# Kernel optimization log

Hardware: AMD Instinct MI355X
Metric: run time of the kernel (lower is better)

The kernel has to match this reference:

```python
import jax, jax.numpy as jnp
import numpy as np

N_NODES = 50000
N_EDGES = 800000
HIDDEN = 128
N_REL = 64
NUM_HEADS = 8
HEAD_DIM = HIDDEN // NUM_HEADS


def setup_inputs() -> dict:
    key = jax.random.key(0)
    ks = jax.random.split(key, 20)
    s = 0.05
    inp = {
        "x": jax.random.normal(ks[0], (N_NODES, HIDDEN), dtype=jnp.float32),
        "timestamps": jax.random.uniform(ks[1], (N_NODES,), dtype=jnp.float32),
        "src": jax.random.randint(ks[2], (N_EDGES,), 0, N_NODES),
        "dst": jax.random.randint(ks[3], (N_EDGES,), 0, N_NODES),
        "edge_type": jax.random.randint(ks[4], (N_EDGES,), 0, N_REL),
        "edge_time": jax.random.uniform(ks[5], (N_EDGES,), dtype=jnp.float32),
        # parameters (torch Linear stored as [in, out] so we use x @ W + b)
        "rel_table": jax.random.normal(ks[6], (N_REL, HIDDEN), dtype=jnp.float32) * s,
        "Wq": jax.random.normal(ks[7], (HIDDEN, HIDDEN), dtype=jnp.float32) * s,
        "bq": jnp.zeros((HIDDEN,), dtype=jnp.float32),
        "Wk": jax.random.normal(ks[8], (HIDDEN, HIDDEN), dtype=jnp.float32) * s,
        "bk": jnp.zeros((HIDDEN,), dtype=jnp.float32),
        "Wv": jax.random.normal(ks[9], (HIDDEN, HIDDEN), dtype=jnp.float32) * s,
        "bv": jnp.zeros((HIDDEN,), dtype=jnp.float32),
        "W1": jax.random.normal(ks[10], (2 * HIDDEN + 1, HIDDEN), dtype=jnp.float32) * s,
        "b1": jnp.zeros((HIDDEN,), dtype=jnp.float32),
        "W2": jax.random.normal(ks[11], (HIDDEN, 1), dtype=jnp.float32) * s,
        "b2": jnp.zeros((1,), dtype=jnp.float32),
        "time_coeff": jnp.array(1.0, dtype=jnp.float32),
    }
    return inp


def reference(x, timestamps, src, dst, edge_type, edge_time, rel_table,
              Wq, bq, Wk, bk, Wv, bv, W1, b1, W2, b2, time_coeff):
    N = x.shape[0]
    # temporal gating
    delta_t = (timestamps[dst] - edge_time) / (jnp.abs(time_coeff) + 1e-9)  # [E]
    time_mask = jax.nn.sigmoid(delta_t)[:, None]                            # [E,1]
    rel_emb = rel_table[edge_type] * time_mask                              # [E,H]
    src_emb = x[src]                                                        # [E,H]
    # dynamic edge weights: MLP([src_emb, rel_emb, time_mask]) -> sigmoid
    weight_input = jnp.concatenate([src_emb, rel_emb, time_mask], axis=-1)  # [E,2H+1]
    h = jax.nn.relu(weight_input @ W1 + b1)
    dynamic_weights = jax.nn.sigmoid(h @ W2 + b2)                           # [E,1]
    message = src_emb * rel_emb * dynamic_weights                           # [E,H]
    # multi-head edge attention keyed by dst
    q = (x[dst] @ Wq + bq).reshape(-1, NUM_HEADS, HEAD_DIM)
    k = (message @ Wk + bk).reshape(-1, NUM_HEADS, HEAD_DIM)
    v = (message @ Wv + bv).reshape(-1, NUM_HEADS, HEAD_DIM)
    scores = (q * k).sum(-1) / (HEAD_DIM ** 0.5)                            # [E,heads]
    # scatter softmax over edges grouped by dst
    seg_max = jax.ops.segment_max(scores, dst, num_segments=N)              # [N,heads]
    e = jnp.exp(scores - seg_max[dst])
    denom = jax.ops.segment_sum(e, dst, num_segments=N)
    attn = e / denom[dst]                                                   # [E,heads]
    out = jax.ops.segment_sum(v * attn[..., None], dst, num_segments=N)     # [N,heads,hd]
    return out.reshape(N, NUM_HEADS * HEAD_DIM)
```

## Files before the change

kernel.cpp:

```cpp
#include <hip/hip_runtime.h>

typedef __bf16 v8bf __attribute__((ext_vector_type(8)));
typedef __bf16 v4bf __attribute__((ext_vector_type(4)));
typedef float  v4f  __attribute__((ext_vector_type(4)));

#define MFMA16x16x32 __builtin_amdgcn_mfma_f32_16x16x32_bf16

#define HIDDEN 128
#define NHEADS 8

__global__ __launch_bounds__(512) void prep_all(
    const float* __restrict__ rel, const float* __restrict__ W1,
    const float* __restrict__ Wk, const float* __restrict__ Wv,
    const float* __restrict__ W2, const int* __restrict__ dst,
    int* __restrict__ count,
    __bf16* __restrict__ mlppre, __bf16* __restrict__ relbf,
    __bf16* __restrict__ wswz, __bf16* __restrict__ w2bf,
    float* __restrict__ outz,
    const float* __restrict__ x, const float* __restrict__ Wq,
    const float* __restrict__ bq, const float* __restrict__ b1,
    __bf16* __restrict__ qbf, __bf16* __restrict__ hpre, __bf16* __restrict__ xbf,
    int N, int E, int hb, int zb, int nz4)
{
  __shared__ __bf16 X[32][136];
  const int b = blockIdx.x;
  if (b < 64) {
    __shared__ float rrow[128];
    const int j = threadIdx.x;
    if (j < 128) rrow[j] = rel[b*HIDDEN + j];
    __syncthreads();
    if (j < 128) {
      float acc = W1[256*HIDDEN + j];
      #pragma unroll 4
      for (int k=0;k<128;k++) acc += rrow[k]*W1[(128+k)*HIDDEN + j];
      mlppre[b*HIDDEN + j] = (__bf16)acc;
      relbf [b*HIDDEN + j] = (__bf16)rrow[j];
    }
    return;
  }
  if (b < 72) {
    int f = (b - 64)*512 + threadIdx.x;
    if (f < 128) w2bf[f] = (__bf16)W2[f];
    if (f >= 2*8*4*64) return;
    int lane = f & 63, kk = (f>>6)&3, c = (f>>8)&7, mat = f>>11;
    const float* W = mat ? Wv : Wk;
    const float scl = mat ? 1.0f : 0.25f;
    int qq = lane>>4, nn = lane&15;
    v8bf o;
    #pragma unroll
    for (int j=0;j<8;j++) o[j] = (__bf16)(W[(kk*32 + qq*8 + j)*HIDDEN + c*16 + nn]*scl);
    *(v8bf*)(wswz + (long)f*8) = o;
    return;
  }
  if (b < 72 + hb) {
    long i = (long)(b - 72)*512 + threadIdx.x;
    long e4 = i*4;
    if (e4 + 3 < E) {
      int4 d = *(const int4*)(dst + e4);
      atomicAdd(&count[d.x], 1);
      atomicAdd(&count[d.y], 1);
      atomicAdd(&count[d.z], 1);
      atomicAdd(&count[d.w], 1);
    } else {
      for (long e = e4; e < E; e++) atomicAdd(&count[dst[e]], 1);
    }
    return;
  }
  if (b < 72 + hb + zb) {
    int idx = (b - 72 - hb)*512 + threadIdx.x;
    if (idx < nz4) ((float4*)outz)[idx] = make_float4(0.f,0.f,0.f,0.f);
    return;
  }
  const int pb = b - (72 + hb + zb), npb = gridDim.x - (72 + hb + zb);
  const int tid = threadIdx.x;
  const int w = tid >> 6, l = tid & 63, qd = l >> 4, ln = l & 15;
  const int col = w*16 + ln;

  v8bf BQ[4], BH[4];
  #pragma unroll
  for (int kk=0; kk<4; kk++) {
    v8bf f, g;
    #pragma unroll
    for (int j=0;j<8;j++){
      f[j] = (__bf16)Wq[(kk*32 + qd*8 + j)*HIDDEN + col];
      g[j] = (__bf16)W1[(kk*32 + qd*8 + j)*HIDDEN + col];
    }
    BQ[kk] = f; BH[kk] = g;
  }
  const float bqv = bq[col], b1v = b1[col];

  const int s = tid >> 4, c8 = (tid & 15)*8;
  for (int n0 = pb*32; n0 < N; n0 += npb*32) {
    __syncthreads();
    int n = n0 + s;
    v8bf xv;
    if (n < N) {
      const float4* xp = (const float4*)(x + (long)n*HIDDEN + c8);
      float4 a = xp[0], b2_ = xp[1];
      xv[0]=(__bf16)a.x; xv[1]=(__bf16)a.y; xv[2]=(__bf16)a.z; xv[3]=(__bf16)a.w;
      xv[4]=(__bf16)b2_.x; xv[5]=(__bf16)b2_.y; xv[6]=(__bf16)b2_.z; xv[7]=(__bf16)b2_.w;
      *(v8bf*)(xbf + (long)n*HIDDEN + c8) = xv;
    } else {
      #pragma unroll
      for (int j=0;j<8;j++) xv[j] = (__bf16)0.f;
    }
    *(v8bf*)&X[s][c8] = xv;
    __syncthreads();

    v4f q0={0.f,0.f,0.f,0.f}, q1={0.f,0.f,0.f,0.f};
    v4f h0={0.f,0.f,0.f,0.f}, h1={0.f,0.f,0.f,0.f};
    #pragma unroll
    for (int kk=0;kk<4;kk++) {
      v8bf a0 = *(const v8bf*)&X[ln][kk*32 + qd*8];
      v8bf a1 = *(const v8bf*)&X[16+ln][kk*32 + qd*8];
      q0 = MFMA16x16x32(a0, BQ[kk], q0, 0,0,0);
      q1 = MFMA16x16x32(a1, BQ[kk], q1, 0,0,0);
      h0 = MFMA16x16x32(a0, BH[kk], h0, 0,0,0);
      h1 = MFMA16x16x32(a1, BH[kk], h1, 0,0,0);
    }
    #pragma unroll
    for (int r=0;r<4;r++) {
      int n_o = n0 + qd*4 + r;
      if (n_o < N) {
        qbf [(long)n_o*HIDDEN + col] = (__bf16)(q0[r] + bqv);
        hpre[(long)n_o*HIDDEN + col] = (__bf16)(h0[r] + b1v);
      }
      int n2 = n0 + 16 + qd*4 + r;
      if (n2 < N) {
        qbf [(long)n2*HIDDEN + col] = (__bf16)(q1[r] + bqv);
        hpre[(long)n2*HIDDEN + col] = (__bf16)(h1[r] + b1v);
      }
    }
  }
}

__global__ __launch_bounds__(1024) void scan_kernel(const int* __restrict__ count,
    int* __restrict__ base, int N)
{
  __shared__ int ssum[1024];
  const int t = threadIdx.x;
  const int chunk = ((N + 4095) >> 12) << 2;
  const int lo = t*chunk, hi = min(lo + chunk, N);
  int s = 0;
  int i = lo;
  for (; i + 3 < hi; i += 4) {
    int4 v = *(const int4*)(count + i);
    s += v.x + v.y + v.z + v.w;
  }
  for (; i < hi; i++) s += count[i];
  ssum[t] = s;
  __syncthreads();
  #pragma unroll
  for (int ofs = 1; ofs < 1024; ofs <<= 1) {
    int v = (t >= ofs) ? ssum[t - ofs] : 0;
    __syncthreads();
    ssum[t] += v;
    __syncthreads();
  }
  int run = (t == 0) ? 0 : ssum[t-1];
  i = lo;
  for (; i + 3 < hi; i += 4) {
    int4 c = *(const int4*)(count + i);
    int4 o;
    o.x = run; o.y = run + c.x; o.z = o.y + c.y; o.w = o.z + c.z;
    *(int4*)(base + i) = o;
    run = o.w + c.w;
  }
  for (; i < hi; i++) { base[i] = run; run += count[i]; }
}

__global__ __launch_bounds__(512) void scat_dw(
    const int* __restrict__ src, const int* __restrict__ dstp,
    const int* __restrict__ etyp, const float* __restrict__ etime,
    const float* __restrict__ ts, const float* __restrict__ tc,
    const __bf16* __restrict__ hpre, const __bf16* __restrict__ mlppre,
    const __bf16* __restrict__ w2bf, const float* __restrict__ b2,
    const int* __restrict__ base, int* __restrict__ cursor,
    int4* __restrict__ meta4, int E)
{
  const int tid = threadIdx.x;
  const int wid = tid >> 6, l = tid & 63;
  const long e0 = ((long)blockIdx.x*8 + wid)*8;
  const int ei = l >> 3, lc = l & 7;

  int s_=0, d_=0, ty_=0; float et_=0.f, tsd_=0.f;
  if (l < 8 && e0 + l < E) {
    long e = e0 + l;
    s_ = src[e]; d_ = dstp[e]; ty_ = etyp[e]; et_ = etime[e]; tsd_ = ts[d_];
  }
  const int sE  = __shfl(s_, ei);
  const int dE  = __shfl(d_, ei);
  const int tyE = __shfl(ty_, ei);
  const float etE  = __shfl(et_, ei);
  const float tsdE = __shfl(tsd_, ei);

  const float invtc = 1.0f / (fabsf(tc[0]) + 1e-9f);
  const float dt = (tsdE - etE) * invtc;
  const float tm = 1.0f/(1.0f + __expf(-dt));

  const v8bf w2a = *(const v8bf*)(w2bf + lc*16);
  const v8bf w2b = *(const v8bf*)(w2bf + lc*16 + 8);
  const __bf16* hp = hpre  + (long)sE *HIDDEN + lc*16;
  const __bf16* mp = mlppre+ (long)tyE*HIDDEN + lc*16;
  v8bf av0 = *(const v8bf*)hp, av1 = *(const v8bf*)(hp + 8);
  v8bf bp0 = *(const v8bf*)mp, bp1 = *(const v8bf*)(mp + 8);

  float z = 0.f;
  #pragma unroll
  for (int j=0;j<8;j++){
    float p0 = (float)av0[j] + tm*(float)bp0[j];
    float p1 = (float)av1[j] + tm*(float)bp1[j];
    z += fmaxf(p0, 0.f)*(float)w2a[j] + fmaxf(p1, 0.f)*(float)w2b[j];
  }
  z += __shfl_xor(z,1); z += __shfl_xor(z,2); z += __shfl_xor(z,4);

  if (lc == 0 && e0 + ei < E) {
    float dw = 1.0f/(1.0f + __expf(-(z + b2[0])));
    int p = base[dE] + atomicAdd(&cursor[dE], 1);
    meta4[p] = make_int4(sE, dE, tyE, __float_as_int(tm * dw));
  }
}

__global__ __launch_bounds__(512, 4) void edge_fused8(
    const int4* __restrict__ meta4,
    const __bf16* __restrict__ xbf, const __bf16* __restrict__ qbf,
    const __bf16* __restrict__ relbf, const __bf16* __restrict__ wswz,
    const float* __restrict__ bk, const float* __restrict__ bv,
    float* __restrict__ out, float* __restrict__ denom, int E, int ntiles)
{
  __shared__ __align__(16) __bf16 MSG[2][4096];

  const int tid = threadIdx.x;
  const int wid = tid >> 6, l = tid & 63, qd = l >> 4, ln = l & 15;
  const int eIdx = wid*4 + qd;

  v8bf bkf[4], bvf[4];
  #pragma unroll
  for (int kk=0;kk<4;kk++){
    bkf[kk] = *(const v8bf*)(wswz +         wid*2048 + kk*512 + (size_t)l*8);
    bvf[kk] = *(const v8bf*)(wswz + 16384 + wid*2048 + kk*512 + (size_t)l*8);
  }
  const float bkc = bk[wid*16 + ln]*0.25f;
  const float bvc = bv[wid*16 + ln];

  const int g = gridDim.x;
  int t = blockIdx.x;
  if (t >= ntiles) return;

  int4 mt = make_int4(0, -1, 0, 0);
  { int e = t*32 + l; if (l < 32 && e < E) mt = meta4[e]; }
  int tn = t + g;
  int4 mtn = make_int4(0, -1, 0, 0);
  if (tn < ntiles) { int e = tn*32 + l; if (l < 32 && e < E) mtn = meta4[e]; }

  float sME = __int_as_float(__shfl(mt.w, eIdx));
  v8bf sv, rv;
  {
    int srcE = __shfl(mt.x, eIdx);
    int tyE  = __shfl(mt.z, eIdx);
    sv = *(const v8bf*)(xbf   + (long)srcE*HIDDEN + ln*8);
    rv = *(const v8bf*)(relbf + (long)tyE *HIDDEN + ln*8);
  }
  int dC[2][4];
  #pragma unroll
  for (int b=0;b<2;b++)
    #pragma unroll
    for (int r=0;r<4;r++) dC[b][r] = __shfl(mt.y, b*16 + qd*4 + r);
  float qA[2][4];
  #pragma unroll
  for (int b=0;b<2;b++)
    #pragma unroll
    for (int r=0;r<4;r++){
      int d = dC[b][r];
      qA[b][r] = (float)qbf[(long)(d<0?0:d)*HIDDEN + wid*16 + ln];
    }

  int p = 0;
  while (true) {
    const int d_m = mt.y;

    int dprev = __shfl(d_m, (l>0)?(l-1):0);
    int flag = (l < 32) && ((l==0) || (d_m != dprev));
    unsigned long long segmask = __ballot(flag);

    const int t2 = tn + g;
    int4 mt2 = make_int4(0, -1, 0, 0);
    if (t2 < ntiles) { int e = t2*32 + l; if (l < 32 && e < E) mt2 = meta4[e]; }

    const float sMN = __int_as_float(__shfl(mtn.w, eIdx));
    const int srcN = __shfl(mtn.x, eIdx);
    const int tyN  = __shfl(mtn.z, eIdx);
    int dN[2][4];
    #pragma unroll
    for (int b=0;b<2;b++)
      #pragma unroll
      for (int r=0;r<4;r++) dN[b][r] = __shfl(mtn.y, b*16 + qd*4 + r);

    {
      char* wbase = (char*)&MSG[p][0] + eIdx*256;
      const int sw = (eIdx & 7) << 4;
      v8bf m;
      #pragma unroll
      for (int j=0;j<8;j++) m[j] = (__bf16)((float)sv[j]*(float)rv[j]*sME);
      *(v8bf*)(wbase + ((ln*16) ^ sw)) = m;
    }

    sv = *(const v8bf*)(xbf   + (long)srcN*HIDDEN + ln*8);
    rv = *(const v8bf*)(relbf + (long)tyN *HIDDEN + ln*8);

    float qB[2][4];
    #pragma unroll
    for (int b=0;b<2;b++)
      #pragma unroll
      for (int r=0;r<4;r++){
        int d = dN[b][r];
        qB[b][r] = (float)qbf[(long)(d<0?0:d)*HIDDEN + wid*16 + ln];
      }

    asm volatile("s_waitcnt lgkmcnt(0)" ::: "memory");
    __builtin_amdgcn_s_barrier();
    __builtin_amdgcn_sched_barrier(0);

    const char* rb = (const char*)&MSG[p][0];
    v4f aK[2], aV[2];
    __builtin_amdgcn_s_setprio(1);
    #pragma unroll
    for (int b=0;b<2;b++){
      const int rrow = b*16 + ln;
      const char* abase = rb + rrow*256;
      const int asw = (rrow & 7) << 4;
      v4f k_ = {0.f,0.f,0.f,0.f}, v_ = {0.f,0.f,0.f,0.f};
      #pragma unroll
      for (int kk=0;kk<4;kk++){
        v8bf a = *(const v8bf*)(abase + ((kk*64 + qd*16) ^ asw));
        k_ = MFMA16x16x32(a, bkf[kk], k_, 0,0,0);
        v_ = MFMA16x16x32(a, bvf[kk], v_, 0,0,0);
      }
      aK[b] = k_; aV[b] = v_;
    }
    __builtin_amdgcn_s_setprio(0);

    float sc[2][4];
    #pragma unroll
    for (int b=0;b<2;b++)
      #pragma unroll
      for (int r=0;r<4;r++) sc[b][r] = (aK[b][r] + bkc)*qA[b][r];
    #pragma unroll
    for (int m=1;m<16;m<<=1){
      #pragma unroll
      for (int b=0;b<2;b++)
        #pragma unroll
        for (int r=0;r<4;r++) sc[b][r] += __shfl_xor(sc[b][r], m);
    }
    float ee[2][4], wv[2][4];
    #pragma unroll
    for (int b=0;b<2;b++)
      #pragma unroll
      for (int r=0;r<4;r++){
        float e_ = __expf(sc[b][r]);
        ee[b][r] = e_;
        wv[b][r] = e_*(aV[b][r] + bvc);
      }

    unsigned long long mm = segmask;
    while (mm){
      int s0 = __ffsll((long long)mm) - 1;
      mm &= mm - 1;
      int s1 = mm ? (__ffsll((long long)mm) - 1) : 32;
      int dseg = __shfl(d_m, s0);
      if (dseg < 0) continue;
      float a0 = 0.f, dn0 = 0.f;
      #pragma unroll
      for (int b=0;b<2;b++)
        #pragma unroll
        for (int r=0;r<4;r++){
          int rw = b*16 + qd*4 + r;
          bool in = (rw >= s0) && (rw < s1);
          a0  += in ? wv[b][r] : 0.f;
          dn0 += in ? ee[b][r] : 0.f;
        }
      a0  += __shfl_xor(a0,16);  a0  += __shfl_xor(a0,32);
      dn0 += __shfl_xor(dn0,16); dn0 += __shfl_xor(dn0,32);
      if (l < 16) atomicAdd(&out[(long)dseg*HIDDEN + wid*16 + ln], a0);
      if (l == 0) atomicAdd(&denom[(long)dseg*NHEADS + wid], dn0);
    }

    if (tn >= ntiles) break;
    t = tn; tn = t2; mt = mtn; mtn = mt2; sME = sMN;
    #pragma unroll
    for (int b=0;b<2;b++)
      #pragma unroll
      for (int r=0;r<4;r++){
        dC[b][r] = dN[b][r];
        qA[b][r] = qB[b][r];
      }
    p ^= 1;
  }
}

__global__ __launch_bounds__(512) void q_kernel(const float* __restrict__ x,
    const float* __restrict__ Wq, const float* __restrict__ bq,
    float* __restrict__ q, int N)
{
  __shared__ __bf16 X[32][136];
  const int tid = threadIdx.x;
  const int w = tid >> 6, l = tid & 63, qd = l >> 4, ln = l & 15;
  const int col = w*16 + ln;
  v8bf B[4];
  #pragma unroll
  for (int kk=0; kk<4; kk++) {
    v8bf f;
    #pragma unroll
    for (int j=0;j<8;j++) f[j] = (__bf16)Wq[(kk*32 + qd*8 + j)*HIDDEN + col];
    B[kk] = f;
  }
  const float bqv = bq[col];
  const int s = tid >> 4, c8 = (tid & 15)*8;
  for (int n0 = blockIdx.x*32; n0 < N; n0 += gridDim.x*32) {
    __syncthreads();
    int n = n0 + s;
    v8bf xv;
    if (n < N) {
      const float4* xp = (const float4*)(x + (long)n*HIDDEN + c8);
      float4 a = xp[0], b = xp[1];
      xv[0]=(__bf16)a.x; xv[1]=(__bf16)a.y; xv[2]=(__bf16)a.z; xv[3]=(__bf16)a.w;
      xv[4]=(__bf16)b.x; xv[5]=(__bf16)b.y; xv[6]=(__bf16)b.z; xv[7]=(__bf16)b.w;
    } else {
      #pragma unroll
      for (int j=0;j<8;j++) xv[j] = (__bf16)0.f;
    }
    *(v8bf*)&X[s][c8] = xv;
    __syncthreads();
    v4f acc0 = {0.f,0.f,0.f,0.f}, acc1 = {0.f,0.f,0.f,0.f};
    #pragma unroll
    for (int kk=0;kk<4;kk++) {
      v8bf a0 = *(const v8bf*)&X[ln][kk*32 + qd*8];
      v8bf a1 = *(const v8bf*)&X[16+ln][kk*32 + qd*8];
      acc0 = MFMA16x16x32(a0, B[kk], acc0, 0,0,0);
      acc1 = MFMA16x16x32(a1, B[kk], acc1, 0,0,0);
    }
    #pragma unroll
    for (int r=0;r<4;r++) {
      int n_o = n0 + qd*4 + r;
      if (n_o < N) q[(long)n_o*HIDDEN + col] = acc0[r] + bqv;
      int n_o2 = n0 + 16 + qd*4 + r;
      if (n_o2 < N) q[(long)n_o2*HIDDEN + col] = acc1[r] + bqv;
    }
  }
}

__global__ __launch_bounds__(512) void edge_atomic(
    const float* __restrict__ x, const float* __restrict__ ts,
    const int* __restrict__ src, const int* __restrict__ dst,
    const int* __restrict__ etyp, const float* __restrict__ etime,
    const float* __restrict__ rel,
    const float* __restrict__ Wk, const float* __restrict__ bk,
    const float* __restrict__ Wv, const float* __restrict__ bv,
    const float* __restrict__ W1, const float* __restrict__ b1,
    const float* __restrict__ W2, const float* __restrict__ b2,
    const float* __restrict__ tc,
    const float* __restrict__ qws, float* __restrict__ denom,
    float* __restrict__ out, int E)
{
  __shared__ __bf16 A[32][264];
  __shared__ __bf16 A2[32][136];
  __shared__ float sW2[128], sb1[128], sw1r[128], sbk[128], sbv[128];
  __shared__ float stm[32], sdw[32];
  __shared__ int   ssrc[32], sdst[32], styp[32];
  __shared__ float dwpart[8][32];
  const int tid = threadIdx.x;
  const int w = tid >> 6, l = tid & 63, qd = l >> 4, ln = l & 15;
  const int col = w*16 + ln;
  v8bf B1[8], BK[4], BV[4];
  #pragma unroll
  for (int kk=0;kk<8;kk++){ v8bf f;
    #pragma unroll
    for (int j=0;j<8;j++) f[j] = (__bf16)W1[(kk*32+qd*8+j)*HIDDEN + col];
    B1[kk]=f; }
  #pragma unroll
  for (int kk=0;kk<4;kk++){ v8bf f,g;
    #pragma unroll
    for (int j=0;j<8;j++){ f[j] = (__bf16)Wk[(kk*32+qd*8+j)*HIDDEN + col];
                           g[j] = (__bf16)Wv[(kk*32+qd*8+j)*HIDDEN + col]; }
    BK[kk]=f; BV[kk]=g; }
  if (tid < 128) {
    sW2[tid]=W2[tid]; sb1[tid]=b1[tid]; sw1r[tid]=W1[256*HIDDEN+tid];
    sbk[tid]=bk[tid]; sbv[tid]=bv[tid];
  }
  const float b2v = b2[0];
  const float invtc = 1.0f / (fabsf(tc[0]) + 1e-9f);
  const int s = tid >> 4, c8 = (tid & 15)*8;
  const int ntiles = (E + 31) >> 5;
  for (int t = blockIdx.x; t < ntiles; t += gridDim.x) {
    const int e0 = t*32;
    __syncthreads();
    if (tid < 32) {
      int e = e0 + tid;
      if (e < E) {
        int d = dst[e];
        ssrc[tid]=src[e]; sdst[tid]=d; styp[tid]=etyp[e];
        float dt = (ts[d] - etime[e]) * invtc;
        stm[tid] = 1.0f/(1.0f+expf(-dt));
      } else { ssrc[tid]=0; sdst[tid]=0; styp[tid]=0; stm[tid]=0.f; }
    }
    __syncthreads();
    {
      const float tmv = stm[s];
      const float4* xp = (const float4*)(x + (long)ssrc[s]*HIDDEN + c8);
      float4 a = xp[0], b = xp[1];
      const float4* rp = (const float4*)(rel + (long)styp[s]*HIDDEN + c8);
      float4 ra = rp[0], rb = rp[1];
      v8bf sv, rv;
      sv[0]=(__bf16)a.x; sv[1]=(__bf16)a.y; sv[2]=(__bf16)a.z; sv[3]=(__bf16)a.w;
      sv[4]=(__bf16)b.x; sv[5]=(__bf16)b.y; sv[6]=(__bf16)b.z; sv[7]=(__bf16)b.w;
      rv[0]=(__bf16)(ra.x*tmv); rv[1]=(__bf16)(ra.y*tmv);
      rv[2]=(__bf16)(ra.z*tmv); rv[3]=(__bf16)(ra.w*tmv);
      rv[4]=(__bf16)(rb.x*tmv); rv[5]=(__bf16)(rb.y*tmv);
      rv[6]=(__bf16)(rb.z*tmv); rv[7]=(__bf16)(rb.w*tmv);
      *(v8bf*)&A[s][c8] = sv;
      *(v8bf*)&A[s][128 + c8] = rv;
    }
    __syncthreads();
    v4f acc0={0.f,0.f,0.f,0.f}, acc1={0.f,0.f,0.f,0.f};
    #pragma unroll
    for (int kk=0;kk<8;kk++){
      v8bf a0 = *(const v8bf*)&A[ln][kk*32 + qd*8];
      v8bf a1 = *(const v8bf*)&A[16+ln][kk*32 + qd*8];
      acc0 = MFMA16x16x32(a0, B1[kk], acc0, 0,0,0);
      acc1 = MFMA16x16x32(a1, B1[kk], acc1, 0,0,0);
    }
    float part[8];
    {
      const float w1rj = sw1r[col], b1j = sb1[col], w2j = sW2[col];
      #pragma unroll
      for (int r=0;r<4;r++){
        int i0 = qd*4 + r, i1 = 16 + qd*4 + r;
        part[r]   = fmaxf(acc0[r] + stm[i0]*w1rj + b1j, 0.f)*w2j;
        part[4+r] = fmaxf(acc1[r] + stm[i1]*w1rj + b1j, 0.f)*w2j;
      }
    }
    #pragma unroll
    for (int m=1;m<16;m<<=1){
      #pragma unroll
      for (int i=0;i<8;i++) part[i] += __shfl_xor(part[i], m, 16);
    }
    if (ln == 0){
      #pragma unroll
      for (int r=0;r<4;r++){ dwpart[w][qd*4+r]=part[r]; dwpart[w][16+qd*4+r]=part[4+r]; }
    }
    __syncthreads();
    if (tid < 32){
      float z = b2v;
      #pragma unroll
      for (int ww=0;ww<8;ww++) z += dwpart[ww][tid];
      sdw[tid] = 1.0f/(1.0f+expf(-z));
    }
    __syncthreads();
    {
      const float dwv = sdw[s];
      v8bf mv;
      #pragma unroll
      for (int i=0;i<8;i++)
        mv[i] = (__bf16)((float)A[s][c8+i]*(float)A[s][128+c8+i]*dwv);
      *(v8bf*)&A2[s][c8] = mv;
    }
    __syncthreads();
    v4f k0={0.f,0.f,0.f,0.f}, k1={0.f,0.f,0.f,0.f};
    v4f v0={0.f,0.f,0.f,0.f}, v1={0.f,0.f,0.f,0.f};
    #pragma unroll
    for (int kk=0;kk<4;kk++){
      v8bf a0 = *(const v8bf*)&A2[ln][kk*32 + qd*8];
      v8bf a1 = *(const v8bf*)&A2[16+ln][kk*32 + qd*8];
      k0 = MFMA16x16x32(a0, BK[kk], k0, 0,0,0);
      k1 = MFMA16x16x32(a1, BK[kk], k1, 0,0,0);
      v0 = MFMA16x16x32(a0, BV[kk], v0, 0,0,0);
      v1 = MFMA16x16x32(a1, BV[kk], v1, 0,0,0);
    }
    float sc[8];
    const float bkj = sbk[col], bvj = sbv[col];
    #pragma unroll
    for (int r=0;r<4;r++){
      int i0 = qd*4 + r, i1 = 16 + qd*4 + r;
      sc[r]   = (k0[r]+bkj)*qws[(long)sdst[i0]*HIDDEN + col];
      sc[4+r] = (k1[r]+bkj)*qws[(long)sdst[i1]*HIDDEN + col];
    }
    #pragma unroll
    for (int m=1;m<16;m<<=1){
      #pragma unroll
      for (int i=0;i<8;i++) sc[i] += __shfl_xor(sc[i], m, 16);
    }
    float ee[8];
    #pragma unroll
    for (int i=0;i<8;i++) ee[i] = expf(sc[i]*0.25f);
    if (ln == 0){
      #pragma unroll
      for (int r=0;r<4;r++){
        int i0 = qd*4 + r, i1 = 16 + qd*4 + r;
        if (e0+i0 < E) atomicAdd(&denom[(long)sdst[i0]*NHEADS + w], ee[r]);
        if (e0+i1 < E) atomicAdd(&denom[(long)sdst[i1]*NHEADS + w], ee[4+r]);
      }
    }
    #pragma unroll
    for (int r=0;r<4;r++){
      int i0 = qd*4 + r, i1 = 16 + qd*4 + r;
      if (e0+i0 < E) atomicAdd(&out[(long)sdst[i0]*HIDDEN + col], ee[r]*(v0[r]+bvj));
      if (e0+i1 < E) atomicAdd(&out[(long)sdst[i1]*HIDDEN + col], ee[4+r]*(v1[r]+bvj));
    }
  }
}

__global__ void fin_kernel(float* __restrict__ out, const float* __restrict__ denom, int N)
{
  int idx = blockIdx.x*blockDim.x + threadIdx.x;
  int total = N*32;
  if (idx < total){
    int n = idx >> 5;
    int h = (idx & 31) >> 2;
    float d = denom[n*8 + h];
    float inv = d > 0.f ? 1.0f/d : 0.f;
    float4* p = (float4*)out + idx;
    float4 v = *p;
    v.x*=inv; v.y*=inv; v.z*=inv; v.w*=inv;
    *p = v;
  }
}

static inline size_t align256(size_t v){ return (v + 255) & ~(size_t)255; }

extern "C" void kernel_launch(void* const* d_in, const int* in_sizes, int n_in,
                              void* d_out, int out_size, void* d_ws, size_t ws_size,
                              hipStream_t stream)
{
  const float* x      = (const float*)d_in[0];
  const float* ts     = (const float*)d_in[1];
  const int*   src    = (const int*)d_in[2];
  const int*   dstp   = (const int*)d_in[3];
  const int*   etyp   = (const int*)d_in[4];
  const float* etime  = (const float*)d_in[5];
  const float* rel    = (const float*)d_in[6];
  const float* Wq     = (const float*)d_in[7];
  const float* bq     = (const float*)d_in[8];
  const float* Wk     = (const float*)d_in[9];
  const float* bk     = (const float*)d_in[10];
  const float* Wv     = (const float*)d_in[11];
  const float* bv     = (const float*)d_in[12];
  const float* W1     = (const float*)d_in[13];
  const float* b1     = (const float*)d_in[14];
  const float* W2     = (const float*)d_in[15];
  const float* b2     = (const float*)d_in[16];
  const float* tc     = (const float*)d_in[17];
  float* out = (float*)d_out;

  const int N = in_sizes[0] / HIDDEN;
  const int E = in_sizes[2];

  char* ws = (char*)d_ws;
  size_t off = 0;
  __bf16* qbf    = (__bf16*)(ws + off); off += align256((size_t)N*HIDDEN*2);
  __bf16* hpre   = (__bf16*)(ws + off); off += align256((size_t)N*HIDDEN*2);
  __bf16* xbf    = (__bf16*)(ws + off); off += align256((size_t)N*HIDDEN*2);
  __bf16* relbf  = (__bf16*)(ws + off); off += align256((size_t)64*HIDDEN*2);
  __bf16* mlppre = (__bf16*)(ws + off); off += align256((size_t)64*HIDDEN*2);
  __bf16* w2bf   = (__bf16*)(ws + off); off += align256((size_t)HIDDEN*2);
  __bf16* wswz   = (__bf16*)(ws + off); off += align256((size_t)4096*8*2);
  size_t zoff = off;
  int*    countp = (int*)(ws + off);    off += align256((size_t)N*4);
  int*    cursor = (int*)(ws + off);    off += align256((size_t)N*4);
  float*  denom  = (float*)(ws + off);  off += align256((size_t)N*NHEADS*4);
  size_t zlen = off - zoff;
  int4*   meta4  = (int4*)(ws + off);   off += align256((size_t)E*16);
  int*    basep  = (int*)(ws + off);    off += align256((size_t)N*4);
  const size_t needed_fast = off;

  if (ws_size >= needed_fast) {
    hipMemsetAsync(ws + zoff, 0, zlen, stream);

    const int hb = (E + 2047)/2048;
    const int nz4 = N*32;
    const int zb = (nz4 + 511)/512;
    prep_all<<<72 + hb + zb + 1024, 512, 0, stream>>>(rel, W1, Wk, Wv, W2,
        dstp, countp, mlppre, relbf, wswz, w2bf, out,
        x, Wq, bq, b1, qbf, hpre, xbf, N, E, hb, zb, nz4);
    scan_kernel<<<1, 1024, 0, stream>>>(countp, basep, N);
    scat_dw<<<(E + 63)/64, 512, 0, stream>>>(src, dstp, etyp, etime, ts, tc,
        hpre, mlppre, w2bf, b2, basep, cursor, meta4, E);

    const int ntiles = (E + 31) >> 5;
    edge_fused8<<<1024, 512, 0, stream>>>(meta4,
        xbf, qbf, relbf, wswz, bk, bv, out, denom, E, ntiles);
    fin_kernel<<<(N*32 + 255)/256, 256, 0, stream>>>(out, denom, N);
  } else {
    float* qws    = (float*)ws;
    float* denom2 = (float*)(ws + align256((size_t)N*HIDDEN*4));
    hipMemsetAsync(out,    0, (size_t)N*HIDDEN*4, stream);
    hipMemsetAsync(denom2, 0, (size_t)N*NHEADS*4, stream);
    q_kernel<<<512, 512, 0, stream>>>(x, Wq, bq, qws, N);
    edge_atomic<<<512, 512, 0, stream>>>(x, ts, src, dstp, etyp, etime, rel,
        Wk, bk, Wv, bv, W1, b1, W2, b2, tc, qws, denom2, out, E);
    fin_kernel<<<(N*32 + 255)/256, 256, 0, stream>>>(out, denom2, N);
  }
}
```

Measured before the change: 451.2 us.

## Overlap node projection GEMM with edge scatter and split dynamic-weight pass

The node-level Q/MLP-pre projection blocks move out of the first prep kernel into a new kernel that also performs the CSR scatter of edge metadata with the time mask. The idea is to let the GEMM overlap with the single-block scan and the scatter instead of running ahead of them. The dynamic-weight MLP then runs as its own pass over the sorted meta4 array, gathering hpre in dst-sorted order and rewriting only the weight field in place. This adds one kernel launch and an extra read and write of meta4, and the scatter no longer waits on the MLP.

```diff
diff --git a/kernel.cpp b/kernel.cpp
--- a/kernel.cpp
+++ b/kernel.cpp
@@ -9,20 +9,15 @@
 #define HIDDEN 128
 #define NHEADS 8
 
-__global__ __launch_bounds__(512) void prep_all(
+__global__ __launch_bounds__(512) void prep_lite(
     const float* __restrict__ rel, const float* __restrict__ W1,
     const float* __restrict__ Wk, const float* __restrict__ Wv,
     const float* __restrict__ W2, const int* __restrict__ dst,
     int* __restrict__ count,
     __bf16* __restrict__ mlppre, __bf16* __restrict__ relbf,
     __bf16* __restrict__ wswz, __bf16* __restrict__ w2bf,
-    float* __restrict__ outz,
-    const float* __restrict__ x, const float* __restrict__ Wq,
-    const float* __restrict__ bq, const float* __restrict__ b1,
-    __bf16* __restrict__ qbf, __bf16* __restrict__ hpre, __bf16* __restrict__ xbf,
-    int N, int E, int hb, int zb, int nz4)
-{
-  __shared__ __bf16 X[32][136];
+    float* __restrict__ outz, int E, int hb, int nz4)
+{
   const int b = blockIdx.x;
   if (b < 64) {
     __shared__ float rrow[128];
@@ -66,12 +61,71 @@
     }
     return;
   }
-  if (b < 72 + hb + zb) {
-    int idx = (b - 72 - hb)*512 + threadIdx.x;
-    if (idx < nz4) ((float4*)outz)[idx] = make_float4(0.f,0.f,0.f,0.f);
+  int idx = (b - 72 - hb)*512 + threadIdx.x;
+  if (idx < nz4) ((float4*)outz)[idx] = make_float4(0.f,0.f,0.f,0.f);
+}
+
+__global__ __launch_bounds__(1024) void scan_kernel(const int* __restrict__ count,
+    int* __restrict__ base, int N)
+{
+  __shared__ int ssum[1024];
+  const int t = threadIdx.x;
+  const int chunk = ((N + 4095) >> 12) << 2;
+  const int lo = t*chunk, hi = min(lo + chunk, N);
+  int s = 0;
+  int i = lo;
+  for (; i + 3 < hi; i += 4) {
+    int4 v = *(const int4*)(count + i);
+    s += v.x + v.y + v.z + v.w;
+  }
+  for (; i < hi; i++) s += count[i];
+  ssum[t] = s;
+  __syncthreads();
+  #pragma unroll
+  for (int ofs = 1; ofs < 1024; ofs <<= 1) {
+    int v = (t >= ofs) ? ssum[t - ofs] : 0;
+    __syncthreads();
+    ssum[t] += v;
+    __syncthreads();
+  }
+  int run = (t == 0) ? 0 : ssum[t-1];
+  i = lo;
+  for (; i + 3 < hi; i += 4) {
+    int4 c = *(const int4*)(count + i);
+    int4 o;
+    o.x = run; o.y = run + c.x; o.z = o.y + c.y; o.w = o.z + c.z;
+    *(int4*)(base + i) = o;
+    run = o.w + c.w;
+  }
+  for (; i < hi; i++) { base[i] = run; run += count[i]; }
+}
+
+__global__ __launch_bounds__(512) void scat_pre(
+    const float* __restrict__ x, const float* __restrict__ Wq,
+    const float* __restrict__ bq, const float* __restrict__ W1,
+    const float* __restrict__ b1,
+    const int* __restrict__ src, const int* __restrict__ dstp,
+    const int* __restrict__ etyp, const float* __restrict__ etime,
+    const float* __restrict__ ts, const float* __restrict__ tc,
+    const int* __restrict__ base, int* __restrict__ cursor,
+    int4* __restrict__ meta4,
+    __bf16* __restrict__ qbf, __bf16* __restrict__ hpre, __bf16* __restrict__ xbf,
+    int N, int E, int SB)
+{
+  __shared__ __bf16 X[32][136];
+  if ((int)blockIdx.x < SB) {
+    int e = blockIdx.x*512 + threadIdx.x;
+    if (e < E) {
+      int d = dstp[e];
+      int pI = base[d] + atomicAdd(&cursor[d], 1);
+      float invtc = 1.0f / (fabsf(tc[0]) + 1e-9f);
+      float dt = (ts[d] - etime[e]) * invtc;
+      float tm = 1.0f/(1.0f + __expf(-dt));
+      meta4[pI] = make_int4(src[e], d, etyp[e], __float_as_int(tm));
+    }
     return;
   }
-  const int pb = b - (72 + hb + zb), npb = gridDim.x - (72 + hb + zb);
+  const int pb = blockIdx.x - SB, npb = gridDim.x - SB;
   const int tid = threadIdx.x;
   const int w = tid >> 6, l = tid & 63, qd = l >> 4, ln = l & 15;
   const int col = w*16 + ln;
@@ -134,69 +188,24 @@
   }
 }
 
-__global__ __launch_bounds__(1024) void scan_kernel(const int* __restrict__ count,
-    int* __restrict__ base, int N)
-{
-  __shared__ int ssum[1024];
-  const int t = threadIdx.x;
-  const int chunk = ((N + 4095) >> 12) << 2;
-  const int lo = t*chunk, hi = min(lo + chunk, N);
-  int s = 0;
-  int i = lo;
-  for (; i + 3 < hi; i += 4) {
-    int4 v = *(const int4*)(count + i);
-    s += v.x + v.y + v.z + v.w;
-  }
-  for (; i < hi; i++) s += count[i];
-  ssum[t] = s;
-  __syncthreads();
-  #pragma unroll
-  for (int ofs = 1; ofs < 1024; ofs <<= 1) {
-    int v = (t >= ofs) ? ssum[t - ofs] : 0;
-    __syncthreads();
-    ssum[t] += v;
-    __syncthreads();
-  }
-  int run = (t == 0) ? 0 : ssum[t-1];
-  i = lo;
-  for (; i + 3 < hi; i += 4) {
-    int4 c = *(const int4*)(count + i);
-    int4 o;
-    o.x = run; o.y = run + c.x; o.z = o.y + c.y; o.w = o.z + c.z;
-    *(int4*)(base + i) = o;
-    run = o.w + c.w;
-  }
-  for (; i < hi; i++) { base[i] = run; run += count[i]; }
-}
-
-__global__ __launch_bounds__(512) void scat_dw(
-    const int* __restrict__ src, const int* __restrict__ dstp,
-    const int* __restrict__ etyp, const float* __restrict__ etime,
-    const float* __restrict__ ts, const float* __restrict__ tc,
+__global__ __launch_bounds__(512) void dw8_kernel(
+    int4* __restrict__ meta4,
     const __bf16* __restrict__ hpre, const __bf16* __restrict__ mlppre,
-    const __bf16* __restrict__ w2bf, const float* __restrict__ b2,
-    const int* __restrict__ base, int* __restrict__ cursor,
-    int4* __restrict__ meta4, int E)
+    const __bf16* __restrict__ w2bf, const float* __restrict__ b2, int E)
 {
   const int tid = threadIdx.x;
   const int wid = tid >> 6, l = tid & 63;
   const long e0 = ((long)blockIdx.x*8 + wid)*8;
   const int ei = l >> 3, lc = l & 7;
 
-  int s_=0, d_=0, ty_=0; float et_=0.f, tsd_=0.f;
+  int s_=0, ty_=0; float tm_=0.f;
   if (l < 8 && e0 + l < E) {
-    long e = e0 + l;
-    s_ = src[e]; d_ = dstp[e]; ty_ = etyp[e]; et_ = etime[e]; tsd_ = ts[d_];
+    int4 mt = meta4[e0 + l];
+    s_ = mt.x; ty_ = mt.z; tm_ = __int_as_float(mt.w);
   }
   const int sE  = __shfl(s_, ei);
-  const int dE  = __shfl(d_, ei);
   const int tyE = __shfl(ty_, ei);
-  const float etE  = __shfl(et_, ei);
-  const float tsdE = __shfl(tsd_, ei);
-
-  const float invtc = 1.0f / (fabsf(tc[0]) + 1e-9f);
-  const float dt = (tsdE - etE) * invtc;
-  const float tm = 1.0f/(1.0f + __expf(-dt));
+  const float tm = __shfl(tm_, ei);
 
   const v8bf w2a = *(const v8bf*)(w2bf + lc*16);
   const v8bf w2b = *(const v8bf*)(w2bf + lc*16 + 8);
@@ -216,8 +225,7 @@
 
   if (lc == 0 && e0 + ei < E) {
     float dw = 1.0f/(1.0f + __expf(-(z + b2[0])));
-    int p = base[dE] + atomicAdd(&cursor[dE], 1);
-    meta4[p] = make_int4(sE, dE, tyE, __float_as_int(tm * dw));
+    ((int*)meta4)[(e0 + ei)*4 + 3] = __float_as_int(tm * dw);
   }
 }
 
@@ -678,12 +686,14 @@
     const int hb = (E + 2047)/2048;
     const int nz4 = N*32;
     const int zb = (nz4 + 511)/512;
-    prep_all<<<72 + hb + zb + 1024, 512, 0, stream>>>(rel, W1, Wk, Wv, W2,
-        dstp, countp, mlppre, relbf, wswz, w2bf, out,
-        x, Wq, bq, b1, qbf, hpre, xbf, N, E, hb, zb, nz4);
+    prep_lite<<<72 + hb + zb, 512, 0, stream>>>(rel, W1, Wk, Wv, W2,
+        dstp, countp, mlppre, relbf, wswz, w2bf, out, E, hb, nz4);
     scan_kernel<<<1, 1024, 0, stream>>>(countp, basep, N);
-    scat_dw<<<(E + 63)/64, 512, 0, stream>>>(src, dstp, etyp, etime, ts, tc,
-        hpre, mlppre, w2bf, b2, basep, cursor, meta4, E);
+    const int SB = (E + 511)/512;
+    scat_pre<<<SB + 1024, 512, 0, stream>>>(x, Wq, bq, W1, b1,
+        src, dstp, etyp, etime, ts, tc, basep, cursor, meta4,
+        qbf, hpre, xbf, N, E, SB);
+    dw8_kernel<<<(E + 63)/64, 512, 0, stream>>>(meta4, hpre, mlppre, w2bf, b2, E);
 
     const int ntiles = (E + 31) >> 5;
     edge_fused8<<<1024, 512, 0, stream>>>(meta4,
```

New measurement: 464.1 us. 2.9% more time.
